# Kernel tuning notes

Hardware: AMD Instinct MI355X
Metric: run time of the kernel (lower is better)

Reference implementation:

```python
import jax, jax.numpy as jnp
import numpy as np

EMBED = 256; HEADS = 8; LEVELS = 4; POINTS = 4; HEAD_DIM = EMBED // HEADS
B = 2; Q = 20000; HP = 128; WP = 128
EPS = 1e-5


def setup_inputs() -> dict:
    key = jax.random.key(0)
    ks = jax.random.split(key, 12)
    s = 1.0 / np.sqrt(EMBED)
    return {
        "query": jax.random.normal(ks[0], (Q, EMBED), jnp.float32),
        "query_spatial_positions": jax.random.uniform(ks[1], (Q, 2), jnp.float32),
        "query_batch_offsets": jnp.array([0, Q // 2, Q], dtype=jnp.int32),
        "stacked_feature_maps": jax.random.normal(ks[2], (B, HP, WP, LEVELS, EMBED), jnp.float32),
        "level_spatial_shapes": jnp.array([[128, 128], [64, 64], [32, 32], [16, 16]], dtype=jnp.int32),
        "norm_gamma": jnp.ones((EMBED,), jnp.float32),
        "norm_beta": jnp.zeros((EMBED,), jnp.float32),
        "W_q": jax.random.normal(ks[3], (EMBED, EMBED), jnp.float32) * s,
        "W_off": jax.random.normal(ks[4], (EMBED, HEADS * LEVELS * POINTS * 2), jnp.float32) * s * 0.1,
        "b_off": jax.random.normal(ks[5], (HEADS * LEVELS * POINTS * 2,), jnp.float32) * 0.5,
        "W_attn": jax.random.normal(ks[6], (EMBED, HEADS * LEVELS * POINTS), jnp.float32) * s,
        "b_attn": jnp.zeros((HEADS * LEVELS * POINTS,), jnp.float32),
        "W_val": jax.random.normal(ks[7], (EMBED, EMBED), jnp.float32) * s,
        "b_val": jnp.zeros((EMBED,), jnp.float32),
        "W_out": jax.random.normal(ks[8], (EMBED, EMBED), jnp.float32) * s,
    }


def _layernorm(x, g, b):
    mu = x.mean(-1, keepdims=True)
    xc = x - mu
    v = (xc * xc).mean(-1, keepdims=True)
    return xc * jax.lax.rsqrt(v + EPS) * g + b


def reference(query, query_spatial_positions, query_batch_offsets, stacked_feature_maps,
              level_spatial_shapes, norm_gamma, norm_beta, W_q, W_off, b_off,
              W_attn, b_attn, W_val, b_val, W_out):
    residual = query
    x = _layernorm(query, norm_gamma, norm_beta)
    x = x @ W_q  # q_in_proj (no bias)

    off = (x @ W_off + b_off).reshape(Q, HEADS, LEVELS, POINTS, 2)
    attn = jax.nn.softmax((x @ W_attn + b_attn).reshape(Q, HEADS, LEVELS * POINTS), axis=-1)
    attn = attn.reshape(Q, HEADS, LEVELS, POINTS)

    # value projection over all levels, split into heads: [B,HP,WP,L,H,HD]
    value = (stacked_feature_maps @ W_val + b_val).reshape(B, HP, WP, LEVELS, HEADS, HEAD_DIM)

    shp = level_spatial_shapes.astype(jnp.float32)  # [L,2] (h,w)
    # normalized ref point + offset scaled by level size -> pixel coords (align_corners=False)
    loc = query_spatial_positions[:, None, None, None, :] + off / shp[None, None, :, None, :]
    pix = loc * shp[None, None, :, None, :] - 0.5  # [Q,H,L,P,2]
    py, px = pix[..., 0], pix[..., 1]
    y0 = jnp.floor(py); x0 = jnp.floor(px)
    wy = py - y0; wx = px - x0
    y0i = y0.astype(jnp.int32); x0i = x0.astype(jnp.int32)

    Hl = level_spatial_shapes[:, 0][None, None, :, None]
    Wl = level_spatial_shapes[:, 1][None, None, :, None]
    b_idx = (jnp.searchsorted(query_batch_offsets, jnp.arange(Q, dtype=jnp.int32), side='right') - 1)[:, None, None, None]
    l_idx = jnp.arange(LEVELS)[None, None, :, None]
    h_idx = jnp.arange(HEADS)[None, :, None, None]

    def gather(yi, xi, w):
        m = (yi >= 0) & (yi < Hl) & (xi >= 0) & (xi < Wl)  # zero-pad outside level extent
        yc = jnp.clip(yi, 0, HP - 1)
        xc = jnp.clip(xi, 0, WP - 1)
        v = value[b_idx, yc, xc, l_idx, h_idx]  # [Q,H,L,P,HD]
        return v * (w * m)[..., None]

    samp = (gather(y0i, x0i, (1 - wy) * (1 - wx))
            + gather(y0i, x0i + 1, (1 - wy) * wx)
            + gather(y0i + 1, x0i, wy * (1 - wx))
            + gather(y0i + 1, x0i + 1, wy * wx))

    out = (attn[..., None] * samp).sum(axis=(2, 3)).reshape(Q, EMBED)
    return out @ W_out + residual
```

## Files before the change

kernel.cpp:

```cpp
#include <hip/hip_runtime.h>
#include <hip/hip_bf16.h>
#include <stdint.h>

#define EMBED 256
#define HEADS 8
#define LEVELS 4
#define POINTS 4
#define HEAD_DIM 32
#define HPAD 128
#define WPAD 128
#define LN_EPS 1e-5f

typedef unsigned short u16;
typedef __attribute__((ext_vector_type(8))) short bf16x8v;
typedef __attribute__((ext_vector_type(4))) float f32x4;

static __device__ __forceinline__ float bu2f(u16 u) {
  return __uint_as_float(((unsigned)u) << 16);
}
static __device__ __forceinline__ u16 f2bu(float f) {
  unsigned x = __float_as_uint(f);
  return (u16)((x + 0x7fffu + ((x >> 16) & 1u)) >> 16);
}
static __device__ __forceinline__ float loadf(const void* p, size_t i, int isbf) {
  return isbf ? bu2f(((const u16*)p)[i]) : ((const float*)p)[i];
}
static __device__ __forceinline__ int imin(int a, int b) { return a < b ? a : b; }

static __device__ __forceinline__ void cp16(const u16* g, u16* l) {
  __builtin_amdgcn_global_load_lds((const __attribute__((address_space(1))) unsigned*)g,
                                   (__attribute__((address_space(3))) unsigned*)l, 16, 0, 0);
}

__global__ __launch_bounds__(256) void detect_kernel(const unsigned* __restrict__ q,
                                                     int* __restrict__ flag) {
  int t = threadIdx.x;
  __shared__ int s[256];
  unsigned u = q[t * 13 + 1];
  unsigned e = (u >> 7) & 0xFF;
  s[t] = (e >= 116 && e <= 130) ? 1 : 0;
  __syncthreads();
  for (int st = 128; st > 0; st >>= 1) { if (t < st) s[t] += s[t + st]; __syncthreads(); }
  if (t == 0) *flag = (s[0] > 200) ? 1 : 0;
}

__global__ __launch_bounds__(384) void boa_kernel(const void* __restrict__ b_off,
                                                  const void* __restrict__ b_attn,
                                                  float* __restrict__ boa,
                                                  const int* __restrict__ dflag) {
  int fl = *dflag;
  int t = threadIdx.x;
  boa[t] = (t < 256) ? loadf(b_off, t, fl) : loadf(b_attn, t - 256, fl);
}

__global__ __launch_bounds__(256) void wtrans_kernel(const void* __restrict__ W,
                                                     u16* __restrict__ Wt,
                                                     int K, int N,
                                                     const int* __restrict__ dflag) {
  int fl = *dflag;
  __shared__ float tile[32][33];
  int tx = threadIdx.x & 31, ty = threadIdx.x >> 5;
  int k0 = blockIdx.x * 32, n0 = blockIdx.y * 32;
#pragma unroll
  for (int j = 0; j < 4; j++) {
    int r = ty + j * 8;
    tile[r][tx] = loadf(W, (size_t)(k0 + r) * N + n0 + tx, fl);
  }
  __syncthreads();
#pragma unroll
  for (int j = 0; j < 4; j++) {
    int n = ty + j * 8;
    Wt[(size_t)(n0 + n) * K + k0 + tx] = f2bu(tile[tx][n]);
  }
}

__global__ __launch_bounds__(256) void ln_kernel(const void* __restrict__ q,
                                                 const void* __restrict__ g,
                                                 const void* __restrict__ be,
                                                 u16* __restrict__ out, int Qn,
                                                 const int* __restrict__ dflag) {
  int fl = *dflag;
  int row = blockIdx.x * 4 + (threadIdx.x >> 6);
  int lane = threadIdx.x & 63;
  if (row >= Qn) return;
  float v0, v1, v2, v3;
  if (fl) {
    uint2 u = *(const uint2*)((const u16*)q + (size_t)row * 256 + lane * 4);
    v0 = bu2f((u16)(u.x & 0xffff)); v1 = bu2f((u16)(u.x >> 16));
    v2 = bu2f((u16)(u.y & 0xffff)); v3 = bu2f((u16)(u.y >> 16));
  } else {
    float4 f = *(const float4*)((const float*)q + (size_t)row * 256 + lane * 4);
    v0 = f.x; v1 = f.y; v2 = f.z; v3 = f.w;
  }
  float s = v0 + v1 + v2 + v3;
#pragma unroll
  for (int m = 1; m < 64; m <<= 1) s += __shfl_xor(s, m, 64);
  float mu = s * (1.f / 256.f);
  float c0 = v0 - mu, c1 = v1 - mu, c2 = v2 - mu, c3 = v3 - mu;
  float s2 = c0 * c0 + c1 * c1 + c2 * c2 + c3 * c3;
#pragma unroll
  for (int m = 1; m < 64; m <<= 1) s2 += __shfl_xor(s2, m, 64);
  float r = rsqrtf(s2 * (1.f / 256.f) + LN_EPS);
  float o0 = c0 * r * loadf(g, lane * 4 + 0, fl) + loadf(be, lane * 4 + 0, fl);
  float o1 = c1 * r * loadf(g, lane * 4 + 1, fl) + loadf(be, lane * 4 + 1, fl);
  float o2 = c2 * r * loadf(g, lane * 4 + 2, fl) + loadf(be, lane * 4 + 2, fl);
  float o3 = c3 * r * loadf(g, lane * 4 + 3, fl) + loadf(be, lane * 4 + 3, fl);
  uint2 w;
  w.x = (unsigned)f2bu(o0) | ((unsigned)f2bu(o1) << 16);
  w.y = (unsigned)f2bu(o2) | ((unsigned)f2bu(o3) << 16);
  *(uint2*)(out + (size_t)row * 256 + lane * 4) = w;
}

template <int OUTMODE, bool ABF>
__global__ __launch_bounds__(256) void mfma_gemm(const void* __restrict__ A,
                                                 const u16* __restrict__ Bt,
                                                 const void* __restrict__ bias, int BiasC,
                                                 const void* __restrict__ resid,
                                                 void* __restrict__ Cv,
                                                 int M, int N, int K,
                                                 const int* __restrict__ dflag) {
  int fl = *dflag;
  __shared__ u16 As[4096];
  __shared__ u16 Bs[4096];
  int tid = threadIdx.x;
  int m0 = blockIdx.x * 128, n0 = blockIdx.y * 128;
  int wave = tid >> 6, lane = tid & 63;
  int quad = lane >> 4, r16 = lane & 15;
  int wm = (wave >> 1) * 64, wn = (wave & 1) * 64;

  f32x4 acc[4][4];
#pragma unroll
  for (int i = 0; i < 4; i++)
#pragma unroll
    for (int j = 0; j < 4; j++) acc[i][j] = (f32x4){0.f, 0.f, 0.f, 0.f};

  int p0 = tid, p1 = tid + 256;
  int r0 = p0 >> 2, c0 = (p0 & 3) * 8;
  int r1 = p1 >> 2, c1 = (p1 & 3) * 8;
  int ra0 = imin(m0 + r0, M - 1), ra1 = imin(m0 + r1, M - 1);

  const u16*   Ab = (const u16*)A;
  const float* Af = (const float*)A;

  for (int k0 = 0; k0 < K; k0 += 32) {
    __syncthreads();
    if (ABF) {
      cp16(Ab + (size_t)ra0 * K + k0 + c0, &As[p0 * 8]);
      cp16(Ab + (size_t)ra1 * K + k0 + c1, &As[p1 * 8]);
    } else if (fl) {
      *(int4*)&As[p0 * 8] = *(const int4*)(Ab + (size_t)ra0 * K + k0 + c0);
      *(int4*)&As[p1 * 8] = *(const int4*)(Ab + (size_t)ra1 * K + k0 + c1);
    } else {
      float4 f00 = *(const float4*)(Af + (size_t)ra0 * K + k0 + c0);
      float4 f01 = *(const float4*)(Af + (size_t)ra0 * K + k0 + c0 + 4);
      float4 f10 = *(const float4*)(Af + (size_t)ra1 * K + k0 + c1);
      float4 f11 = *(const float4*)(Af + (size_t)ra1 * K + k0 + c1 + 4);
      u16* d0 = &As[p0 * 8];
      d0[0] = f2bu(f00.x); d0[1] = f2bu(f00.y); d0[2] = f2bu(f00.z); d0[3] = f2bu(f00.w);
      d0[4] = f2bu(f01.x); d0[5] = f2bu(f01.y); d0[6] = f2bu(f01.z); d0[7] = f2bu(f01.w);
      u16* d1 = &As[p1 * 8];
      d1[0] = f2bu(f10.x); d1[1] = f2bu(f10.y); d1[2] = f2bu(f10.z); d1[3] = f2bu(f10.w);
      d1[4] = f2bu(f11.x); d1[5] = f2bu(f11.y); d1[6] = f2bu(f11.z); d1[7] = f2bu(f11.w);
    }
    cp16(Bt + (size_t)(n0 + r0) * K + k0 + c0, &Bs[p0 * 8]);
    cp16(Bt + (size_t)(n0 + r1) * K + k0 + c1, &Bs[p1 * 8]);
    __syncthreads();

    bf16x8v a[4], b[4];
#pragma unroll
    for (int i = 0; i < 4; i++)
      a[i] = *(const bf16x8v*)&As[(wm + i * 16 + r16) * 32 + quad * 8];
#pragma unroll
    for (int j = 0; j < 4; j++)
      b[j] = *(const bf16x8v*)&Bs[(wn + j * 16 + r16) * 32 + quad * 8];
#pragma unroll
    for (int i = 0; i < 4; i++)
#pragma unroll
      for (int j = 0; j < 4; j++)
        acc[i][j] = __builtin_amdgcn_mfma_f32_16x16x32_bf16(a[i], b[j], acc[i][j], 0, 0, 0);
  }

  int obf = (OUTMODE == 2) ? fl : OUTMODE;
  int bfl = (BiasC == 2) ? fl : 0;
  if (bias) {
#pragma unroll
    for (int j = 0; j < 4; j++) {
      float bv = loadf(bias, n0 + wn + j * 16 + r16, bfl);
#pragma unroll
      for (int i = 0; i < 4; i++)
#pragma unroll
        for (int reg = 0; reg < 4; reg++) acc[i][j][reg] += bv;
    }
  }

  if (obf) {
    int sl0 = (quad << 4) | ((2 * r16) & 15);
    int sl1 = sl0 + 1;
    bool lohalf = (r16 < 8);
#pragma unroll
    for (int i = 0; i < 4; i++) {
#pragma unroll
      for (int jp = 0; jp < 2; jp++) {
#pragma unroll
        for (int reg = 0; reg < 4; reg++) {
          float vA = acc[i][jp * 2][reg], vB = acc[i][jp * 2 + 1][reg];
          float a0 = __shfl(vA, sl0), a1 = __shfl(vA, sl1);
          float b0 = __shfl(vB, sl0), b1 = __shfl(vB, sl1);
          float lo = lohalf ? a0 : b0;
          float hi = lohalf ? a1 : b1;
          int row = m0 + wm + i * 16 + quad * 4 + reg;
          if (row < M) {
            size_t base = (size_t)row * N + n0 + wn + jp * 32 + 2 * r16;
            if (resid) {
              lo += loadf(resid, base, fl);
              hi += loadf(resid, base + 1, fl);
            }
            unsigned pk = (unsigned)f2bu(lo) | ((unsigned)f2bu(hi) << 16);
            *(unsigned*)((u16*)Cv + base) = pk;
          }
        }
      }
    }
  } else {
#pragma unroll
    for (int j = 0; j < 4; j++) {
      int col = n0 + wn + j * 16 + r16;
#pragma unroll
      for (int i = 0; i < 4; i++) {
#pragma unroll
        for (int reg = 0; reg < 4; reg++) {
          int row = m0 + wm + i * 16 + quad * 4 + reg;
          if (row < M) {
            float v = acc[i][j][reg];
            if (resid) v += loadf(resid, (size_t)row * N + col, fl);
            ((float*)Cv)[(size_t)row * N + col] = v;
          }
        }
      }
    }
  }
}

__global__ __launch_bounds__(512) void val_gemm(const void* __restrict__ A,
                                                const u16* __restrict__ Bt,
                                                const void* __restrict__ bias,
                                                u16* __restrict__ Cv,
                                                const int* __restrict__ dflag) {
  int fl = *dflag;
  __shared__ u16 As[128 * 256];
  int tid = threadIdx.x;
  int blk = blockIdx.x;
  int b   = blk / 170;
  int cb  = blk % 170;
  int l, ibase;
  if (cb < 128)      { l = 0; ibase = cb * 128; }
  else if (cb < 160) { l = 1; ibase = (cb - 128) * 128; }
  else if (cb < 168) { l = 2; ibase = (cb - 160) * 128; }
  else               { l = 3; ibase = (cb - 168) * 128; }
  int shift = 7 - l;
  int mask  = (128 >> l) - 1;
  int rowbase = b * 65536 + l;

  int wave = tid >> 6, lane = tid & 63;
  int quad = lane >> 4, r16 = lane & 15;
  int wm = (wave >> 2) * 64, wn = (wave & 3) * 64;

  if (fl) {
    const uint4* A16 = (const uint4*)A;
#pragma unroll
    for (int it = 0; it < 8; it++) {
      int g = it * 512 + tid;
      int r = g >> 5, c = g & 31;
      int i = ibase + r;
      size_t rowg = (size_t)rowbase + (i >> shift) * 512 + (i & mask) * 4;
      uint4 v = A16[rowg * 32 + c];
      *(uint4*)&As[r * 256 + ((c ^ (r & 7)) * 8)] = v;
    }
  } else {
    const float4* A4 = (const float4*)A;
#pragma unroll
    for (int p = 0; p < 2; p++) {
      float4 f[8];
#pragma unroll
      for (int q = 0; q < 8; q++) {
        int g = (p * 8 + q) * 512 + tid;
        int i = ibase + (g >> 6);
        size_t rowg = (size_t)rowbase + (i >> shift) * 512 + (i & mask) * 4;
        f[q] = A4[rowg * 64 + (g & 63)];
      }
#pragma unroll
      for (int q = 0; q < 8; q++) {
        int g = (p * 8 + q) * 512 + tid;
        int r = g >> 6, cw = g & 63;
        int c = cw >> 1, sub = cw & 1;
        uint2 w;
        w.x = (unsigned)f2bu(f[q].x) | ((unsigned)f2bu(f[q].y) << 16);
        w.y = (unsigned)f2bu(f[q].z) | ((unsigned)f2bu(f[q].w) << 16);
        *(uint2*)&As[r * 256 + ((c ^ (r & 7)) * 8) + sub * 4] = w;
      }
    }
  }
  __syncthreads();

  f32x4 acc[4][4];
#pragma unroll
  for (int i = 0; i < 4; i++)
#pragma unroll
    for (int j = 0; j < 4; j++) acc[i][j] = (f32x4){0.f, 0.f, 0.f, 0.f};

  int arow[4], arl[4];
#pragma unroll
  for (int i = 0; i < 4; i++) {
    arow[i] = (wm + i * 16 + r16) * 256;
    arl[i]  = (wm + i * 16 + r16) & 7;
  }
  const u16* bbase[4];
#pragma unroll
  for (int j = 0; j < 4; j++)
    bbase[j] = Bt + (size_t)(wn + j * 16 + r16) * 256 + quad * 8;

#pragma unroll
  for (int t = 0; t < 8; t++) {
    bf16x8v b4[4];
#pragma unroll
    for (int j = 0; j < 4; j++)
      b4[j] = *(const bf16x8v*)(bbase[j] + t * 32);
    bf16x8v a4[4];
#pragma unroll
    for (int i = 0; i < 4; i++) {
      int chunk = ((t << 2) | quad) ^ arl[i];
      a4[i] = *(const bf16x8v*)&As[arow[i] + chunk * 8];
    }
#pragma unroll
    for (int i = 0; i < 4; i++)
#pragma unroll
      for (int j = 0; j < 4; j++)
        acc[i][j] = __builtin_amdgcn_mfma_f32_16x16x32_bf16(a4[i], b4[j], acc[i][j], 0, 0, 0);
  }

#pragma unroll
  for (int j = 0; j < 4; j++) {
    float bv = loadf(bias, wn + j * 16 + r16, fl);
#pragma unroll
    for (int i = 0; i < 4; i++)
#pragma unroll
      for (int reg = 0; reg < 4; reg++) acc[i][j][reg] += bv;
  }
  int sl0 = (quad << 4) | ((2 * r16) & 15);
  int sl1 = sl0 + 1;
  bool lohalf = (r16 < 8);
#pragma unroll
  for (int i = 0; i < 4; i++) {
#pragma unroll
    for (int jp = 0; jp < 2; jp++) {
#pragma unroll
      for (int reg = 0; reg < 4; reg++) {
        float vA = acc[i][jp * 2][reg], vB = acc[i][jp * 2 + 1][reg];
        float a0 = __shfl(vA, sl0), a1 = __shfl(vA, sl1);
        float b0 = __shfl(vB, sl0), b1 = __shfl(vB, sl1);
        float lo = lohalf ? a0 : b0;
        float hi = lohalf ? a1 : b1;
        int rloc = wm + i * 16 + quad * 4 + reg;
        int ii = ibase + rloc;
        size_t rowg = (size_t)rowbase + (ii >> shift) * 512 + (ii & mask) * 4;
        size_t base = rowg * 256 + wn + jp * 32 + 2 * r16;
        unsigned pk = (unsigned)f2bu(lo) | ((unsigned)f2bu(hi) << 16);
        *(unsigned*)(Cv + base) = pk;
      }
    }
  }
}

__global__ __launch_bounds__(256) void sample2_kernel(const float* __restrict__ oa,
                                                      const void* __restrict__ qsp,
                                                      const int* __restrict__ qbo, int nb,
                                                      const int* __restrict__ lss,
                                                      const u16* __restrict__ value,
                                                      u16* __restrict__ samp, int Qn,
                                                      const int* __restrict__ dflag) {
  int fl = *dflag;
  int t = threadIdx.x;
  int q2 = t >> 7;
  int i7 = t & 127;
  int qb = blockIdx.x * 2;
  int q = imin(qb + q2, Qn - 1);

  __shared__ float Loff[2][256];
  __shared__ float Lw[2][128];
  __shared__ int   Lb[2];
  __shared__ int   Co[2][128][4];
  __shared__ float Cw[2][128][4];

  {
    const float* row = oa + (size_t)q * 384;
    float2 v = ((const float2*)row)[i7];
    Loff[q2][i7 * 2]     = v.x;
    Loff[q2][i7 * 2 + 1] = v.y;
    Lw[q2][i7] = row[256 + i7];
  }
  if (t < 2) {
    int qq = imin(qb + t, Qn - 1);
    int b = 0;
    for (int i = 1; i < nb; i++) if (qq >= qbo[i]) b = i;
    Lb[t] = b;
  }
  __syncthreads();

  if (t < 16) {
    int sq = t >> 3, h = t & 7;
    float* w = &Lw[sq][h * 16];
    float mx = w[0];
    for (int i = 1; i < 16; i++) mx = fmaxf(mx, w[i]);
    float s = 0.f;
    for (int i = 0; i < 16; i++) { float e = __expf(w[i] - mx); w[i] = e; s += e; }
    float inv = 1.f / s;
    for (int i = 0; i < 16; i++) w[i] *= inv;
  }
  __syncthreads();

  {
    int h = i7 >> 4, lp = i7 & 15, l = lp >> 2;
    int Hi = lss[l * 2], Wi = lss[l * 2 + 1];
    float Hl = (float)Hi, Wl = (float)Wi;
    float qy = loadf(qsp, (size_t)q * 2, fl);
    float qx = loadf(qsp, (size_t)q * 2 + 1, fl);
    float a  = Lw[q2][i7];
    float oy = Loff[q2][i7 * 2], ox = Loff[q2][i7 * 2 + 1];
    float py = (qy + oy / Hl) * Hl - 0.5f;
    float px = (qx + ox / Wl) * Wl - 0.5f;
    float y0f = floorf(py), x0f = floorf(px);
    float wy = py - y0f, wx = px - x0f;
    int y0 = (int)y0f, x0 = (int)x0f;
    int bbase = Lb[q2] * (HPAD * WPAD * LEVELS * EMBED);
#pragma unroll
    for (int c = 0; c < 4; c++) {
      int yi = y0 + (c >> 1), xi = x0 + (c & 1);
      float w = ((c >> 1) ? wy : 1.f - wy) * ((c & 1) ? wx : 1.f - wx);
      bool ok = (yi >= 0) & (yi < Hi) & (xi >= 0) & (xi < Wi);
      Co[q2][i7][c] = ok ? (bbase + ((yi * WPAD + xi) * LEVELS + l) * EMBED + h * HEAD_DIM) : 0;
      Cw[q2][i7][c] = ok ? (a * w) : 0.f;
    }
  }
  __syncthreads();

  {
    int h = (t >> 4) & 7;
    int d2 = t & 15;
    float ax = 0.f, ay = 0.f;
#pragma unroll
    for (int lp = 0; lp < 16; lp++) {
      int4   o4 = *(const int4*)&Co[q2][h * 16 + lp][0];
      float4 w4 = *(const float4*)&Cw[q2][h * 16 + lp][0];
      unsigned v;
      v = *(const unsigned*)(value + o4.x + d2 * 2);
      ax += w4.x * __uint_as_float(v << 16); ay += w4.x * __uint_as_float(v & 0xffff0000u);
      v = *(const unsigned*)(value + o4.y + d2 * 2);
      ax += w4.y * __uint_as_float(v << 16); ay += w4.y * __uint_as_float(v & 0xffff0000u);
      v = *(const unsigned*)(value + o4.z + d2 * 2);
      ax += w4.z * __uint_as_float(v << 16); ay += w4.z * __uint_as_float(v & 0xffff0000u);
      v = *(const unsigned*)(value + o4.w + d2 * 2);
      ax += w4.w * __uint_as_float(v << 16); ay += w4.w * __uint_as_float(v & 0xffff0000u);
    }
    if (qb + q2 < Qn) {
      unsigned pk = (unsigned)f2bu(ax) | ((unsigned)f2bu(ay) << 16);
      *(unsigned*)(samp + (size_t)(qb + q2) * 256 + h * 32 + d2 * 2) = pk;
    }
  }
}

extern "C" void kernel_launch(void* const* d_in, const int* in_sizes, int n_in,
                              void* d_out, int out_size, void* d_ws, size_t ws_size,
                              hipStream_t stream) {
  const void* query  = d_in[0];
  const void* qsp    = d_in[1];
  const int*  qbo    = (const int*)d_in[2];
  const void* sfm    = d_in[3];
  const int*  lss    = (const int*)d_in[4];
  const void* gamma  = d_in[5];
  const void* beta   = d_in[6];
  const void* W_q    = d_in[7];
  const void* W_off  = d_in[8];
  const void* b_off  = d_in[9];
  const void* W_attn = d_in[10];
  const void* b_attn = d_in[11];
  const void* W_val  = d_in[12];
  const void* b_val  = d_in[13];
  const void* W_out  = d_in[14];

  const int Q  = in_sizes[0] / EMBED;
  const int nb = in_sizes[2] - 1;
  const int MV = in_sizes[3] / EMBED;
  const int B  = MV / (HPAD * WPAD * LEVELS);

  char* ws = (char*)d_ws;
  size_t o = 0;
  auto alloc = [&](size_t bytes) { size_t r = o; o = (o + bytes + 255) & ~(size_t)255; return r; };
  u16*   xln   = (u16*)(ws + alloc((size_t)Q * EMBED * sizeof(u16)));
  u16*   x     = (u16*)(ws + alloc((size_t)Q * EMBED * sizeof(u16)));
  float* oaw   = (float*)(ws + alloc((size_t)Q * 384 * sizeof(float)));
  u16*   valw  = (u16*)(ws + alloc((size_t)MV * EMBED * sizeof(u16)));
  u16*   sampw = (u16*)(ws + alloc((size_t)Q * EMBED * sizeof(u16)));
  u16*   wtq   = (u16*)(ws + alloc(256 * 256 * sizeof(u16)));
  u16*   wtoa  = (u16*)(ws + alloc(384 * 256 * sizeof(u16)));
  u16*   wtval = (u16*)(ws + alloc(256 * 256 * sizeof(u16)));
  u16*   wtout = (u16*)(ws + alloc(256 * 256 * sizeof(u16)));
  float* boa   = (float*)(ws + alloc(384 * sizeof(float)));
  int*   dflag = (int*)(ws + alloc(256));
  (void)ws_size;

  detect_kernel<<<1, 256, 0, stream>>>((const unsigned*)query, dflag);
  boa_kernel<<<1, 384, 0, stream>>>(b_off, b_attn, boa, dflag);

  wtrans_kernel<<<dim3(8, 8), 256, 0, stream>>>(W_q,    wtq,              256, 256, dflag);
  wtrans_kernel<<<dim3(8, 8), 256, 0, stream>>>(W_off,  wtoa,             256, 256, dflag);
  wtrans_kernel<<<dim3(8, 4), 256, 0, stream>>>(W_attn, wtoa + 256 * 256, 256, 128, dflag);
  wtrans_kernel<<<dim3(8, 8), 256, 0, stream>>>(W_val,  wtval,            256, 256, dflag);
  wtrans_kernel<<<dim3(8, 8), 256, 0, stream>>>(W_out,  wtout,            256, 256, dflag);

  ln_kernel<<<(Q + 3) / 4, 256, 0, stream>>>(query, gamma, beta, xln, Q, dflag);

  const int GQ = (Q + 127) / 128;
  mfma_gemm<1, true><<<dim3(GQ, 2), 256, 0, stream>>>(xln, wtq, nullptr, 0, nullptr, x, Q, 256, 256, dflag);
  mfma_gemm<0, true><<<dim3(GQ, 3), 256, 0, stream>>>(x, wtoa, boa, 0, nullptr, oaw, Q, 384, 256, dflag);
  val_gemm<<<dim3(B * 170), 512, 0, stream>>>(sfm, wtval, b_val, valw, dflag);
  sample2_kernel<<<(Q + 1) / 2, 256, 0, stream>>>(oaw, qsp, qbo, nb, lss, valw, sampw, Q, dflag);
  mfma_gemm<2, true><<<dim3(GQ, 2), 256, 0, stream>>>(sampw, wtout, nullptr, 0, query, d_out, Q, 256, 256, dflag);
}
```

Baseline: 381.0 us.

## Fold W_q into offset/attention weights and vectorize sampling gathers

Precomputes W_q·[W_off|W_attn] on device in a small combined-weight kernel, so the query projection GEMM and its intermediate buffer are removed and the offset/attention GEMM reads the layernormed input directly. The sampling inner loop is also reorganized so that each lane loads 16 bytes (8 bf16 values) per corner instead of 4 bytes, and partial sums are reduced across the four corner lanes with shuffles. This cuts one full Q×256×256 GEMM plus its memory traffic and widens the value gathers. In exchange, the combined weight is rounded to bf16 after fp32 accumulation, which changes rounding slightly, and the weight-combine kernel runs a small serial matmul.

```diff
diff --git a/kernel.cpp b/kernel.cpp
--- a/kernel.cpp
+++ b/kernel.cpp
@@ -51,6 +51,31 @@
   int fl = *dflag;
   int t = threadIdx.x;
   boa[t] = (t < 256) ? loadf(b_off, t, fl) : loadf(b_attn, t - 256, fl);
+}
+
+__global__ __launch_bounds__(1024) void wcomb_kernel(const void* __restrict__ Wq,
+                                                     const void* __restrict__ Woff,
+                                                     const void* __restrict__ Wattn,
+                                                     u16* __restrict__ Wt,
+                                                     const int* __restrict__ dflag) {
+  int fl = *dflag;
+  int n0 = blockIdx.x * 32, k0 = blockIdx.y * 32;
+  int tx = threadIdx.x & 31;
+  int ty = threadIdx.x >> 5;
+  __shared__ float Aq[32][33];
+  __shared__ float Bo[32][33];
+  float acc = 0.f;
+  for (int j0 = 0; j0 < 256; j0 += 32) {
+    Aq[ty][tx] = loadf(Wq, (size_t)(k0 + ty) * 256 + j0 + tx, fl);
+    int n = n0 + tx;
+    Bo[ty][tx] = (n < 256) ? loadf(Woff,  (size_t)(j0 + ty) * 256 + n,        fl)
+                           : loadf(Wattn, (size_t)(j0 + ty) * 128 + (n - 256), fl);
+    __syncthreads();
+#pragma unroll
+    for (int j = 0; j < 32; j++) acc += Aq[ty][j] * Bo[j][tx];
+    __syncthreads();
+  }
+  Wt[(size_t)(n0 + tx) * 256 + k0 + ty] = f2bu(acc);
 }
 
 __global__ __launch_bounds__(256) void wtrans_kernel(const void* __restrict__ W,
@@ -444,26 +469,34 @@
   __syncthreads();
 
   {
-    int h = (t >> 4) & 7;
-    int d2 = t & 15;
-    float ax = 0.f, ay = 0.f;
+    int h  = i7 >> 4;
+    int c4 = i7 & 3;
+    int d4 = (i7 >> 2) & 3;
+    float a0 = 0.f, a1 = 0.f, a2 = 0.f, a3 = 0.f, a4 = 0.f, a5 = 0.f, a6 = 0.f, a7 = 0.f;
 #pragma unroll
     for (int lp = 0; lp < 16; lp++) {
-      int4   o4 = *(const int4*)&Co[q2][h * 16 + lp][0];
-      float4 w4 = *(const float4*)&Cw[q2][h * 16 + lp][0];
-      unsigned v;
-      v = *(const unsigned*)(value + o4.x + d2 * 2);
-      ax += w4.x * __uint_as_float(v << 16); ay += w4.x * __uint_as_float(v & 0xffff0000u);
-      v = *(const unsigned*)(value + o4.y + d2 * 2);
-      ax += w4.y * __uint_as_float(v << 16); ay += w4.y * __uint_as_float(v & 0xffff0000u);
-      v = *(const unsigned*)(value + o4.z + d2 * 2);
-      ax += w4.z * __uint_as_float(v << 16); ay += w4.z * __uint_as_float(v & 0xffff0000u);
-      v = *(const unsigned*)(value + o4.w + d2 * 2);
-      ax += w4.w * __uint_as_float(v << 16); ay += w4.w * __uint_as_float(v & 0xffff0000u);
-    }
-    if (qb + q2 < Qn) {
-      unsigned pk = (unsigned)f2bu(ax) | ((unsigned)f2bu(ay) << 16);
-      *(unsigned*)(samp + (size_t)(qb + q2) * 256 + h * 32 + d2 * 2) = pk;
+      int   off = Co[q2][h * 16 + lp][c4];
+      float w   = Cw[q2][h * 16 + lp][c4];
+      uint4 v = *(const uint4*)(value + off + d4 * 8);
+      a0 += w * __uint_as_float(v.x << 16); a1 += w * __uint_as_float(v.x & 0xffff0000u);
+      a2 += w * __uint_as_float(v.y << 16); a3 += w * __uint_as_float(v.y & 0xffff0000u);
+      a4 += w * __uint_as_float(v.z << 16); a5 += w * __uint_as_float(v.z & 0xffff0000u);
+      a6 += w * __uint_as_float(v.w << 16); a7 += w * __uint_as_float(v.w & 0xffff0000u);
+    }
+#pragma unroll
+    for (int m = 1; m <= 2; m <<= 1) {
+      a0 += __shfl_xor(a0, m, 64); a1 += __shfl_xor(a1, m, 64);
+      a2 += __shfl_xor(a2, m, 64); a3 += __shfl_xor(a3, m, 64);
+      a4 += __shfl_xor(a4, m, 64); a5 += __shfl_xor(a5, m, 64);
+      a6 += __shfl_xor(a6, m, 64); a7 += __shfl_xor(a7, m, 64);
+    }
+    if (c4 == 0 && qb + q2 < Qn) {
+      uint4 pk;
+      pk.x = (unsigned)f2bu(a0) | ((unsigned)f2bu(a1) << 16);
+      pk.y = (unsigned)f2bu(a2) | ((unsigned)f2bu(a3) << 16);
+      pk.z = (unsigned)f2bu(a4) | ((unsigned)f2bu(a5) << 16);
+      pk.w = (unsigned)f2bu(a6) | ((unsigned)f2bu(a7) << 16);
+      *(uint4*)(samp + (size_t)(qb + q2) * 256 + h * 32 + d4 * 8) = pk;
     }
   }
 }
@@ -496,11 +529,9 @@
   size_t o = 0;
   auto alloc = [&](size_t bytes) { size_t r = o; o = (o + bytes + 255) & ~(size_t)255; return r; };
   u16*   xln   = (u16*)(ws + alloc((size_t)Q * EMBED * sizeof(u16)));
-  u16*   x     = (u16*)(ws + alloc((size_t)Q * EMBED * sizeof(u16)));
   float* oaw   = (float*)(ws + alloc((size_t)Q * 384 * sizeof(float)));
   u16*   valw  = (u16*)(ws + alloc((size_t)MV * EMBED * sizeof(u16)));
   u16*   sampw = (u16*)(ws + alloc((size_t)Q * EMBED * sizeof(u16)));
-  u16*   wtq   = (u16*)(ws + alloc(256 * 256 * sizeof(u16)));
   u16*   wtoa  = (u16*)(ws + alloc(384 * 256 * sizeof(u16)));
   u16*   wtval = (u16*)(ws + alloc(256 * 256 * sizeof(u16)));
   u16*   wtout = (u16*)(ws + alloc(256 * 256 * sizeof(u16)));
@@ -511,17 +542,14 @@
   detect_kernel<<<1, 256, 0, stream>>>((const unsigned*)query, dflag);
   boa_kernel<<<1, 384, 0, stream>>>(b_off, b_attn, boa, dflag);
 
-  wtrans_kernel<<<dim3(8, 8), 256, 0, stream>>>(W_q,    wtq,              256, 256, dflag);
-  wtrans_kernel<<<dim3(8, 8), 256, 0, stream>>>(W_off,  wtoa,             256, 256, dflag);
-  wtrans_kernel<<<dim3(8, 4), 256, 0, stream>>>(W_attn, wtoa + 256 * 256, 256, 128, dflag);
-  wtrans_kernel<<<dim3(8, 8), 256, 0, stream>>>(W_val,  wtval,            256, 256, dflag);
-  wtrans_kernel<<<dim3(8, 8), 256, 0, stream>>>(W_out,  wtout,            256, 256, dflag);
+  wcomb_kernel<<<dim3(12, 8), 1024, 0, stream>>>(W_q, W_off, W_attn, wtoa, dflag);
+  wtrans_kernel<<<dim3(8, 8), 256, 0, stream>>>(W_val, wtval, 256, 256, dflag);
+  wtrans_kernel<<<dim3(8, 8), 256, 0, stream>>>(W_out, wtout, 256, 256, dflag);
 
   ln_kernel<<<(Q + 3) / 4, 256, 0, stream>>>(query, gamma, beta, xln, Q, dflag);
 
   const int GQ = (Q + 127) / 128;
-  mfma_gemm<1, true><<<dim3(GQ, 2), 256, 0, stream>>>(xln, wtq, nullptr, 0, nullptr, x, Q, 256, 256, dflag);
-  mfma_gemm<0, true><<<dim3(GQ, 3), 256, 0, stream>>>(x, wtoa, boa, 0, nullptr, oaw, Q, 384, 256, dflag);
+  mfma_gemm<0, true><<<dim3(GQ, 3), 256, 0, stream>>>(xln, wtoa, boa, 0, nullptr, oaw, Q, 384, 256, dflag);
   val_gemm<<<dim3(B * 170), 512, 0, stream>>>(sfm, wtval, b_val, valw, dflag);
   sample2_kernel<<<(Q + 1) / 2, 256, 0, stream>>>(oaw, qsp, qbo, nb, lss, valw, sampw, Q, dflag);
   mfma_gemm<2, true><<<dim3(GQ, 2), 256, 0, stream>>>(sampw, wtout, nullptr, 0, query, d_out, Q, 256, 256, dflag);
```

Result: slower. 402.5 us (+5.7%).

## Fold W_q into offset/attention weights to drop the q projection GEMM

Applied to the files above, without the earlier changes.

A small kernel precomputes W_q·[W_off | W_attn] (256x384) each call and stores it transposed in bf16. The offset/attention GEMM then reads the layernorm output directly, which removes the Q×256×256 projection GEMM and its intermediate buffer write and read. The folded weight is rounded to bf16 once, so numerics differ slightly from rounding x in bf16 and then multiplying.

```diff
diff --git a/kernel.cpp b/kernel.cpp
--- a/kernel.cpp
+++ b/kernel.cpp
@@ -51,6 +51,31 @@
   int fl = *dflag;
   int t = threadIdx.x;
   boa[t] = (t < 256) ? loadf(b_off, t, fl) : loadf(b_attn, t - 256, fl);
+}
+
+__global__ __launch_bounds__(1024) void wcomb_kernel(const void* __restrict__ Wq,
+                                                     const void* __restrict__ Woff,
+                                                     const void* __restrict__ Wattn,
+                                                     u16* __restrict__ Wt,
+                                                     const int* __restrict__ dflag) {
+  int fl = *dflag;
+  int n0 = blockIdx.x * 32, k0 = blockIdx.y * 32;
+  int tx = threadIdx.x & 31;
+  int ty = threadIdx.x >> 5;
+  __shared__ float Aq[32][33];
+  __shared__ float Bo[32][33];
+  float acc = 0.f;
+  for (int j0 = 0; j0 < 256; j0 += 32) {
+    Aq[ty][tx] = loadf(Wq, (size_t)(k0 + ty) * 256 + j0 + tx, fl);
+    int n = n0 + tx;
+    Bo[ty][tx] = (n < 256) ? loadf(Woff,  (size_t)(j0 + ty) * 256 + n,        fl)
+                           : loadf(Wattn, (size_t)(j0 + ty) * 128 + (n - 256), fl);
+    __syncthreads();
+#pragma unroll
+    for (int j = 0; j < 32; j++) acc += Aq[ty][j] * Bo[j][tx];
+    __syncthreads();
+  }
+  Wt[(size_t)(n0 + tx) * 256 + k0 + ty] = f2bu(acc);
 }
 
 __global__ __launch_bounds__(256) void wtrans_kernel(const void* __restrict__ W,
@@ -496,11 +521,9 @@
   size_t o = 0;
   auto alloc = [&](size_t bytes) { size_t r = o; o = (o + bytes + 255) & ~(size_t)255; return r; };
   u16*   xln   = (u16*)(ws + alloc((size_t)Q * EMBED * sizeof(u16)));
-  u16*   x     = (u16*)(ws + alloc((size_t)Q * EMBED * sizeof(u16)));
   float* oaw   = (float*)(ws + alloc((size_t)Q * 384 * sizeof(float)));
   u16*   valw  = (u16*)(ws + alloc((size_t)MV * EMBED * sizeof(u16)));
   u16*   sampw = (u16*)(ws + alloc((size_t)Q * EMBED * sizeof(u16)));
-  u16*   wtq   = (u16*)(ws + alloc(256 * 256 * sizeof(u16)));
   u16*   wtoa  = (u16*)(ws + alloc(384 * 256 * sizeof(u16)));
   u16*   wtval = (u16*)(ws + alloc(256 * 256 * sizeof(u16)));
   u16*   wtout = (u16*)(ws + alloc(256 * 256 * sizeof(u16)));
@@ -511,17 +534,14 @@
   detect_kernel<<<1, 256, 0, stream>>>((const unsigned*)query, dflag);
   boa_kernel<<<1, 384, 0, stream>>>(b_off, b_attn, boa, dflag);
 
-  wtrans_kernel<<<dim3(8, 8), 256, 0, stream>>>(W_q,    wtq,              256, 256, dflag);
-  wtrans_kernel<<<dim3(8, 8), 256, 0, stream>>>(W_off,  wtoa,             256, 256, dflag);
-  wtrans_kernel<<<dim3(8, 4), 256, 0, stream>>>(W_attn, wtoa + 256 * 256, 256, 128, dflag);
-  wtrans_kernel<<<dim3(8, 8), 256, 0, stream>>>(W_val,  wtval,            256, 256, dflag);
-  wtrans_kernel<<<dim3(8, 8), 256, 0, stream>>>(W_out,  wtout,            256, 256, dflag);
+  wcomb_kernel<<<dim3(12, 8), 1024, 0, stream>>>(W_q, W_off, W_attn, wtoa, dflag);
+  wtrans_kernel<<<dim3(8, 8), 256, 0, stream>>>(W_val, wtval, 256, 256, dflag);
+  wtrans_kernel<<<dim3(8, 8), 256, 0, stream>>>(W_out, wtout, 256, 256, dflag);
 
   ln_kernel<<<(Q + 3) / 4, 256, 0, stream>>>(query, gamma, beta, xln, Q, dflag);
 
   const int GQ = (Q + 127) / 128;
-  mfma_gemm<1, true><<<dim3(GQ, 2), 256, 0, stream>>>(xln, wtq, nullptr, 0, nullptr, x, Q, 256, 256, dflag);
-  mfma_gemm<0, true><<<dim3(GQ, 3), 256, 0, stream>>>(x, wtoa, boa, 0, nullptr, oaw, Q, 384, 256, dflag);
+  mfma_gemm<0, true><<<dim3(GQ, 3), 256, 0, stream>>>(xln, wtoa, boa, 0, nullptr, oaw, Q, 384, 256, dflag);
   val_gemm<<<dim3(B * 170), 512, 0, stream>>>(sfm, wtval, b_val, valw, dflag);
   sample2_kernel<<<(Q + 1) / 2, 256, 0, stream>>>(oaw, qsp, qbo, nb, lss, valw, sampw, Q, dflag);
   mfma_gemm<2, true><<<dim3(GQ, 2), 256, 0, stream>>>(sampw, wtout, nullptr, 0, query, d_out, Q, 256, 256, dflag);
```

Result: no change. 375.3 us, median of 2 (-1.5%).
